# Kernel tuning notes

Measured on AMD Instinct MI355X. Metric: run time of the kernel, lower is better.

## Reference

```python
import jax, jax.numpy as jnp
import numpy as np

SENTINEL = 24635
NUM_ENTITIES = 24636
EMB_DIM = 128


def setup_inputs() -> dict:
    key = jax.random.key(0)
    ks = jax.random.split(key, 6)
    B, L = 4096, 50
    return {
        "encoded_context_embs": jax.random.normal(ks[0], (B, 1024), jnp.float32),
        "ent_embs": jax.random.normal(ks[1], (NUM_ENTITIES, EMB_DIM), jnp.float32) * 0.02,
        "W1": jax.random.normal(ks[2], (768, 1024), jnp.float32) * 0.02,
        "W2": jax.random.normal(ks[3], (512, 768), jnp.float32) * 0.02,
        "W3": jax.random.normal(ks[4], (128, 512), jnp.float32) * 0.02,
        "ent_list": jax.random.randint(ks[5], (B, L), 0, NUM_ENTITIES, jnp.int64),
    }


def reference(encoded_context_embs, ent_embs, W1, W2, W3, ent_list):
    # --- ragged gather + masked mean with sentinel early-exit ---
    # valid[b, l] == 1 iff no sentinel appeared at positions <= l (prefix-AND)
    not_sent = (ent_list != SENTINEL).astype(ent_embs.dtype)   # [B, L]
    valid = jnp.cumprod(not_sent, axis=1)                      # [B, L]
    gathered = ent_embs[ent_list]                              # [B, L, D]
    cnt = valid.sum(axis=1)                                    # [B]
    summed = jnp.einsum("bl,bld->bd", valid, gathered)        # [B, D]
    mean = summed / jnp.maximum(cnt, 1.0)[:, None]
    # sentinel at position 0 -> fall back to the sentinel embedding
    user_embs = jnp.where((cnt == 0)[:, None], ent_embs[SENTINEL][None, :], mean)

    # --- MLP on pooled context: 1024 -> 768 -> 512 -> 128 ---
    x = jax.nn.relu(encoded_context_embs @ W1.T)
    x = jax.nn.relu(x @ W2.T)
    q = x @ W3.T                                               # [B, 128]

    # --- cross attention: query=q, key=value=user_embs ---
    scale = 1.0 / jnp.sqrt(jnp.asarray(q.shape[-1], q.dtype))
    scores = (q @ user_embs.T) * scale                         # [B, B]
    weights = jax.nn.softmax(scores, axis=-1)
    return weights @ user_embs                                 # [B, 128]
```

## Files before the change

### kernel.cpp

```cpp
#include <hip/hip_runtime.h>
#include <hip/hip_bf16.h>

#define SENTINEL 24635

typedef unsigned char f8_t;
using bf16x8  = __attribute__((ext_vector_type(8))) __bf16;
using bf16x2  = __attribute__((ext_vector_type(2))) __bf16;
using floatx4 = __attribute__((ext_vector_type(4))) float;

__device__ inline int pack4_fp8(float4 a, float s) {
  int w = __builtin_amdgcn_cvt_pk_fp8_f32(a.x * s, a.y * s, 0, false);
  return __builtin_amdgcn_cvt_pk_fp8_f32(a.z * s, a.w * s, w, true);
}

__device__ inline void store_fp8x8(f8_t* d, float4 a, float4 b, float s) {
  int2 v; v.x = pack4_fp8(a, s); v.y = pack4_fp8(b, s);
  *(int2*)d = v;
}

__device__ inline void gll16(const void* g, void* l) {
  __builtin_amdgcn_global_load_lds(
      (const __attribute__((address_space(1))) unsigned int*)g,
      (__attribute__((address_space(3))) unsigned int*)l, 16, 0, 0);
}

__global__ __launch_bounds__(256) void prep_kernel(
    const float* __restrict__ s0, f8_t* __restrict__ d0,
    const float* __restrict__ s1, f8_t* __restrict__ d1,
    const float* __restrict__ s2, f8_t* __restrict__ d2,
    const float* __restrict__ s3, f8_t* __restrict__ d3,
    const float* __restrict__ ent, const int* __restrict__ ent_list,
    __bf16* __restrict__ user_n) {
  if (blockIdx.x < 2656) {
    int g = blockIdx.x * 256 + threadIdx.x;
    const float* s; f8_t* d; int i; float sc;
    if (g < 524288)      { s = s0; d = d0; i = g;          sc = 1.f;  }
    else if (g < 622592) { s = s1; d = d1; i = g - 524288; sc = 16.f; }
    else if (g < 671744) { s = s2; d = d2; i = g - 622592; sc = 16.f; }
    else if (g < 679936) { s = s3; d = d3; i = g - 671744; sc = 16.f; }
    else return;
    i *= 8;
    float4 a = *(const float4*)(s + i);
    float4 b = *(const float4*)(s + i + 4);
    store_fp8x8(d + i, a, b, sc);
    return;
  }
  const int b = (blockIdx.x - 2656) * 4 + (threadIdx.x >> 6);
  const int lane = threadIdx.x & 63;
  int myidx = (lane < 50) ? ent_list[b * 50 + lane] : 0;
  unsigned long long m = __ballot(lane < 50 && myidx == SENTINEL);
  const int cnt = (m == 0) ? 50 : (int)__builtin_ctzll(m);

  float sx = 0.f, sy = 0.f;
  for (int l0 = 0; l0 < 50; l0 += 10) {
    if (l0 >= cnt) break;
    float2 e[10];
#pragma unroll
    for (int j = 0; j < 10; ++j) {
      int idx = __shfl(myidx, l0 + j);
      e[j] = *(const float2*)(ent + (size_t)idx * 128 + lane * 2);
    }
#pragma unroll
    for (int j = 0; j < 10; ++j) {
      if (l0 + j < cnt) { sx += e[j].x; sy += e[j].y; }
    }
  }
  float vx, vy;
  if (cnt == 0) {
    float2 e = *(const float2*)(ent + (size_t)SENTINEL * 128 + lane * 2);
    vx = e.x; vy = e.y;
  } else {
    float inv = 1.f / (float)cnt;
    vx = sx * inv; vy = sy * inv;
  }
  bf16x2 o; o[0] = (__bf16)vx; o[1] = (__bf16)vy;
  *(bf16x2*)(user_n + (size_t)b * 128 + lane * 2) = o;
}

template <int WR, int WC, int MT, int NT, int RELU, bool OUT_BF16>
__device__ inline void gemm_body_f8(const f8_t* __restrict__ A,
                                    const f8_t* __restrict__ W,
                                    void* __restrict__ Cout,
                                    int M, int N, int K, int bn0, int bm0,
                                    char* lds) {
  constexpr int BM = WR * MT * 16;
  constexpr int BN = WC * NT * 16;
  auto As = (f8_t (*)[BM][32])lds;
  auto Bs = (f8_t (*)[BN][32])(lds + (size_t)2 * BM * 32);
  const int tid  = threadIdx.x;
  const int w    = tid >> 6;
  const int lane = tid & 63;
  const int quad = lane >> 4;
  const int l16  = lane & 15;
  const int wr   = w / WC;
  const int wc   = w % WC;
  const int lrow = lane >> 1;
  const int lcol = (lane & 1) * 16;

  floatx4 acc[MT][NT];
#pragma unroll
  for (int mt = 0; mt < MT; ++mt)
#pragma unroll
    for (int nt = 0; nt < NT; ++nt) acc[mt][nt] = (floatx4){0.f, 0.f, 0.f, 0.f};

  constexpr int nAc = 2 * (BM / 32);
  constexpr int nBc = 2 * (BN / 32);
  for (int k0 = 0; k0 < K; k0 += 64) {
    __syncthreads();
#pragma unroll
    for (int c = w; c < nAc; c += 4) {
      int s = c / (BM / 32);
      int r = (c % (BM / 32)) * 32;
      gll16(A + (size_t)(bm0 + r + lrow) * K + k0 + s * 32 + lcol, &As[s][r][0]);
    }
#pragma unroll
    for (int c = w; c < nBc; c += 4) {
      int s = c / (BN / 32);
      int r = (c % (BN / 32)) * 32;
      gll16(W + (size_t)(bn0 + r + lrow) * K + k0 + s * 32 + lcol, &Bs[s][r][0]);
    }
    __syncthreads();
#pragma unroll
    for (int s = 0; s < 2; ++s) {
      long af[MT], bfr[NT];
#pragma unroll
      for (int mt = 0; mt < MT; ++mt)
        af[mt] = *(const long*)&As[s][wr * (MT * 16) + mt * 16 + l16][quad * 8];
#pragma unroll
      for (int nt = 0; nt < NT; ++nt)
        bfr[nt] = *(const long*)&Bs[s][wc * (NT * 16) + nt * 16 + l16][quad * 8];
#pragma unroll
      for (int mt = 0; mt < MT; ++mt)
#pragma unroll
        for (int nt = 0; nt < NT; ++nt)
          acc[mt][nt] = __builtin_amdgcn_mfma_f32_16x16x32_fp8_fp8(
              af[mt], bfr[nt], acc[mt][nt], 0, 0, 0);
    }
  }

  const float osc = 0.0625f;
#pragma unroll
  for (int mt = 0; mt < MT; ++mt) {
    const int row0 = bm0 + wr * (MT * 16) + mt * 16 + quad * 4;
#pragma unroll
    for (int nt = 0; nt < NT; ++nt) {
      const int col = bn0 + wc * (NT * 16) + nt * 16 + l16;
#pragma unroll
      for (int r = 0; r < 4; ++r) {
        float v = acc[mt][nt][r] * osc;
        if (RELU) v = fmaxf(v, 0.f);
        if (OUT_BF16) {
          ((__bf16*)Cout)[(size_t)(row0 + r) * N + col] = (__bf16)v;
        } else {
          int p = __builtin_amdgcn_cvt_pk_fp8_f32(v, v, 0, false);
          ((f8_t*)Cout)[(size_t)(row0 + r) * N + col] = (f8_t)(p & 0xff);
        }
      }
    }
  }
}

template <int WR, int WC, int MT, int NT, int RELU, bool OUT_BF16>
__global__ __launch_bounds__(256) void gemm_f8(const f8_t* __restrict__ A,
                                               const f8_t* __restrict__ W,
                                               void* __restrict__ C,
                                               int M, int N, int K) {
  __shared__ char lds[(size_t)2 * ((WR * MT * 16) + (WC * NT * 16)) * 32];
  gemm_body_f8<WR, WC, MT, NT, RELU, OUT_BF16>(
      A, W, C, M, N, K, blockIdx.x * (WC * NT * 16), blockIdx.y * (WR * MT * 16),
      lds);
}

__global__ __launch_bounds__(256) void gemm1_tr(const f8_t* __restrict__ A,
                                                const f8_t* __restrict__ W,
                                                f8_t* __restrict__ C,
                                                const __bf16* __restrict__ un,
                                                __bf16* __restrict__ ut) {
  __shared__ char lds[10240];
  const int bx = blockIdx.x;
  if (bx < 512) {
    gemm_body_f8<2, 2, 2, 3, 1, false>(A, W, C, 4096, 768, 1024,
                                       (bx % 8) * 96, (bx / 8) * 64, lds);
    return;
  }
  const int idx = bx - 512;
  const int r0 = (idx & 63) * 64;
  const int c0 = (idx >> 6) * 64;
  auto T = (__bf16 (*)[72])lds;
  const int tid = threadIdx.x;
#pragma unroll
  for (int p = 0; p < 2; ++p) {
    int r = (tid >> 3) + p * 32;
    int c = (tid & 7) * 8;
    *(bf16x8*)&T[r][c] = *(const bf16x8*)(un + (size_t)(r0 + r) * 128 + c0 + c);
  }
  __syncthreads();
#pragma unroll
  for (int p = 0; p < 2; ++p) {
    int c = (tid >> 3) + p * 32;
    int r = (tid & 7) * 8;
    bf16x8 v;
#pragma unroll
    for (int j = 0; j < 8; ++j) v[j] = T[r + j][c];
    *(bf16x8*)(ut + (size_t)(c0 + c) * 4096 + r0 + r) = v;
  }
}

__global__ __launch_bounds__(256) void flash_attn(const __bf16* __restrict__ Q,
                                                  const __bf16* __restrict__ Un_g,
                                                  const __bf16* __restrict__ Ut_g,
                                                  __bf16* __restrict__ O_part,
                                                  float* __restrict__ lp) {
  __shared__ __bf16 Un[64][136];
  __shared__ __bf16 Ut[128][72];
  __shared__ __bf16 Ps[4][32][72];
  const int tid  = threadIdx.x;
  const int w    = tid >> 6;
  const int lane = tid & 63;
  const int quad = lane >> 4;
  const int l16  = lane & 15;
  const int qrow0 = blockIdx.x * 128;
  const int split = blockIdx.y;
  const float scale = 0.08838834764831845f;

  bf16x8 aq[2][4];
#pragma unroll
  for (int mt = 0; mt < 2; ++mt)
#pragma unroll
    for (int c = 0; c < 4; ++c)
      aq[mt][c] = *(const bf16x8*)(Q + (size_t)(qrow0 + w * 32 + mt * 16 + l16) * 128 +
                                   c * 32 + quad * 8);

  floatx4 o[2][8];
#pragma unroll
  for (int mt = 0; mt < 2; ++mt)
#pragma unroll
    for (int t = 0; t < 8; ++t) o[mt][t] = (floatx4){0.f, 0.f, 0.f, 0.f};
  float lsum[2][4] = {{0.f, 0.f, 0.f, 0.f}, {0.f, 0.f, 0.f, 0.f}};

  for (int chunk = 0; chunk < 4; ++chunk) {
    const int key0 = (split * 4 + chunk) * 64;
    __syncthreads();
#pragma unroll
    for (int p = 0; p < 4; ++p) {
      int r = (tid >> 4) + p * 16;
      int c = (tid & 15) * 8;
      *(bf16x8*)&Un[r][c] = *(const bf16x8*)(Un_g + (size_t)(key0 + r) * 128 + c);
    }
#pragma unroll
    for (int p = 0; p < 4; ++p) {
      int d = (tid >> 3) + p * 32;
      int kk = (tid & 7) * 8;
      *(bf16x8*)&Ut[d][kk] = *(const bf16x8*)(Ut_g + (size_t)d * 4096 + key0 + kk);
    }
    __syncthreads();

#pragma unroll
    for (int t = 0; t < 4; ++t) {
      bf16x8 bk[4];
#pragma unroll
      for (int c = 0; c < 4; ++c)
        bk[c] = *(const bf16x8*)&Un[t * 16 + l16][c * 32 + quad * 8];
      floatx4 s0 = (floatx4){0.f, 0.f, 0.f, 0.f};
      floatx4 s1 = (floatx4){0.f, 0.f, 0.f, 0.f};
#pragma unroll
      for (int c = 0; c < 4; ++c) {
        s0 = __builtin_amdgcn_mfma_f32_16x16x32_bf16(aq[0][c], bk[c], s0, 0, 0, 0);
        s1 = __builtin_amdgcn_mfma_f32_16x16x32_bf16(aq[1][c], bk[c], s1, 0, 0, 0);
      }
#pragma unroll
      for (int r = 0; r < 4; ++r) {
        float p0 = __expf(s0[r] * scale);
        float p1 = __expf(s1[r] * scale);
        lsum[0][r] += p0;
        lsum[1][r] += p1;
        Ps[w][quad * 4 + r][t * 16 + l16] = (__bf16)p0;
        Ps[w][16 + quad * 4 + r][t * 16 + l16] = (__bf16)p1;
      }
    }

#pragma unroll
    for (int c2 = 0; c2 < 2; ++c2) {
      bf16x8 ap0 = *(const bf16x8*)&Ps[w][l16][c2 * 32 + quad * 8];
      bf16x8 ap1 = *(const bf16x8*)&Ps[w][16 + l16][c2 * 32 + quad * 8];
#pragma unroll
      for (int dt = 0; dt < 8; ++dt) {
        bf16x8 bv = *(const bf16x8*)&Ut[dt * 16 + l16][c2 * 32 + quad * 8];
        o[0][dt] = __builtin_amdgcn_mfma_f32_16x16x32_bf16(ap0, bv, o[0][dt], 0, 0, 0);
        o[1][dt] = __builtin_amdgcn_mfma_f32_16x16x32_bf16(ap1, bv, o[1][dt], 0, 0, 0);
      }
    }
  }

#pragma unroll
  for (int mt = 0; mt < 2; ++mt)
#pragma unroll
    for (int r = 0; r < 4; ++r) {
      float v = lsum[mt][r];
      v += __shfl_xor(v, 1);
      v += __shfl_xor(v, 2);
      v += __shfl_xor(v, 4);
      v += __shfl_xor(v, 8);
      lsum[mt][r] = v;
    }

  __bf16* Ob = O_part + (size_t)split * 524288;
#pragma unroll
  for (int mt = 0; mt < 2; ++mt) {
    const int row0 = qrow0 + w * 32 + mt * 16 + quad * 4;
#pragma unroll
    for (int dt = 0; dt < 8; ++dt) {
#pragma unroll
      for (int r = 0; r < 4; ++r) {
        Ob[(size_t)(row0 + r) * 128 + dt * 16 + l16] = (__bf16)o[mt][dt][r];
      }
    }
    if (l16 == 0) {
#pragma unroll
      for (int r = 0; r < 4; ++r) lp[(size_t)split * 4096 + row0 + r] = lsum[mt][r];
    }
  }
}

__global__ __launch_bounds__(256) void combine_kernel(const __bf16* __restrict__ Op,
                                                      const float* __restrict__ lp,
                                                      float* __restrict__ out) {
  const int i = (blockIdx.x * 256 + threadIdx.x) * 8;
  const int row = i >> 7;
  float num[8] = {0.f, 0.f, 0.f, 0.f, 0.f, 0.f, 0.f, 0.f};
  float den = 0.f;
#pragma unroll
  for (int s = 0; s < 16; ++s) {
    bf16x8 v = *(const bf16x8*)(Op + (size_t)s * 524288 + i);
#pragma unroll
    for (int j = 0; j < 8; ++j) num[j] += (float)v[j];
    den += lp[(size_t)s * 4096 + row];
  }
  float inv = 1.f / den;
  float4 r0 = {num[0] * inv, num[1] * inv, num[2] * inv, num[3] * inv};
  float4 r1 = {num[4] * inv, num[5] * inv, num[6] * inv, num[7] * inv};
  *(float4*)(out + i) = r0;
  *(float4*)(out + i + 4) = r1;
}

extern "C" void kernel_launch(void* const* d_in, const int* in_sizes, int n_in,
                              void* d_out, int out_size, void* d_ws, size_t ws_size,
                              hipStream_t stream) {
  (void)in_sizes; (void)n_in; (void)out_size; (void)ws_size;
  const float* ctx      = (const float*)d_in[0];
  const float* ent_embs = (const float*)d_in[1];
  const float* W1       = (const float*)d_in[2];
  const float* W2       = (const float*)d_in[3];
  const float* W3       = (const float*)d_in[4];
  const int*   ent_list = (const int*)d_in[5];
  float* out = (float*)d_out;

  char* base = (char*)d_ws;
  __bf16* user_n = (__bf16*)(base);
  __bf16* user_t = (__bf16*)(base + (1ull << 20));
  __bf16* qb     = (__bf16*)(base + (2ull << 20));
  float*  lp     = (float*)(base + (3ull << 20));
  f8_t*   ctxb   = (f8_t*)(base + (4ull << 20));
  f8_t*   W1b    = (f8_t*)(base + (8ull << 20));
  f8_t*   W2b    = (f8_t*)(base + 9175040ull);
  f8_t*   W3b    = (f8_t*)(base + 9568256ull);
  f8_t*   x1b    = (f8_t*)(base + (10ull << 20));
  f8_t*   x2b    = (f8_t*)(base + (13ull << 20));
  __bf16* O_part = (__bf16*)(base + (15ull << 20));

  prep_kernel<<<3680, 256, 0, stream>>>(ctx, ctxb, W1, W1b, W2, W2b, W3, W3b,
                                        ent_embs, ent_list, user_n);
  gemm1_tr<<<640, 256, 0, stream>>>(ctxb, W1b, x1b, user_n, user_t);
  gemm_f8<2, 2, 2, 2, 1, false><<<dim3(8, 64), 256, 0, stream>>>(
      x1b, W2b, x2b, 4096, 512, 768);
  gemm_f8<2, 2, 1, 1, 0, true><<<dim3(4, 128), 256, 0, stream>>>(
      x2b, W3b, qb, 4096, 128, 512);
  flash_attn<<<dim3(32, 16), 256, 0, stream>>>(qb, user_n, user_t, O_part, lp);
  combine_kernel<<<256, 256, 0, stream>>>(O_part, lp, out);
}
```

Baseline: 156.2 us.

## Prefetch attention key chunks into registers and move W2/W3 conversion into gemm1

The flash-attention loop now loads the next 64-key chunk of Un/Ut from global memory into registers while computing on the current chunk, then stores it to LDS after a barrier. This hides global load latency behind the MFMA work. MFMA sections are wrapped in s_setprio raises. The W2/W3 fp8 conversion moves from the prep kernel into extra blocks of the gemm1 launch, shrinking prep and overlapping that conversion with the first GEMM. The cost is higher register pressure from the prefetch buffers and an extra barrier per chunk.

```diff
diff --git a/kernel.cpp b/kernel.cpp
--- a/kernel.cpp
+++ b/kernel.cpp
@@ -27,25 +27,20 @@
 __global__ __launch_bounds__(256) void prep_kernel(
     const float* __restrict__ s0, f8_t* __restrict__ d0,
     const float* __restrict__ s1, f8_t* __restrict__ d1,
-    const float* __restrict__ s2, f8_t* __restrict__ d2,
-    const float* __restrict__ s3, f8_t* __restrict__ d3,
     const float* __restrict__ ent, const int* __restrict__ ent_list,
     __bf16* __restrict__ user_n) {
-  if (blockIdx.x < 2656) {
+  if (blockIdx.x < 2432) {
     int g = blockIdx.x * 256 + threadIdx.x;
     const float* s; f8_t* d; int i; float sc;
     if (g < 524288)      { s = s0; d = d0; i = g;          sc = 1.f;  }
-    else if (g < 622592) { s = s1; d = d1; i = g - 524288; sc = 16.f; }
-    else if (g < 671744) { s = s2; d = d2; i = g - 622592; sc = 16.f; }
-    else if (g < 679936) { s = s3; d = d3; i = g - 671744; sc = 16.f; }
-    else return;
+    else                 { s = s1; d = d1; i = g - 524288; sc = 16.f; }
     i *= 8;
     float4 a = *(const float4*)(s + i);
     float4 b = *(const float4*)(s + i + 4);
     store_fp8x8(d + i, a, b, sc);
     return;
   }
-  const int b = (blockIdx.x - 2656) * 4 + (threadIdx.x >> 6);
+  const int b = (blockIdx.x - 2432) * 4 + (threadIdx.x >> 6);
   const int lane = threadIdx.x & 63;
   int myidx = (lane < 50) ? ent_list[b * 50 + lane] : 0;
   unsigned long long m = __ballot(lane < 50 && myidx == SENTINEL);
@@ -175,12 +170,27 @@
                                                 const f8_t* __restrict__ W,
                                                 f8_t* __restrict__ C,
                                                 const __bf16* __restrict__ un,
-                                                __bf16* __restrict__ ut) {
+                                                __bf16* __restrict__ ut,
+                                                const float* __restrict__ s2,
+                                                f8_t* __restrict__ d2,
+                                                const float* __restrict__ s3,
+                                                f8_t* __restrict__ d3) {
   __shared__ char lds[10240];
   const int bx = blockIdx.x;
   if (bx < 512) {
     gemm_body_f8<2, 2, 2, 3, 1, false>(A, W, C, 4096, 768, 1024,
                                        (bx % 8) * 96, (bx / 8) * 64, lds);
+    return;
+  }
+  if (bx >= 640) {
+    int g = (bx - 640) * 256 + threadIdx.x;
+    const float* s; f8_t* d; int i;
+    if (g < 49152) { s = s2; d = d2; i = g; }
+    else           { s = s3; d = d3; i = g - 49152; }
+    i *= 8;
+    float4 a = *(const float4*)(s + i);
+    float4 b = *(const float4*)(s + i + 4);
+    store_fp8x8(d + i, a, b, 16.f);
     return;
   }
   const int idx = bx - 512;
@@ -238,22 +248,34 @@
     for (int t = 0; t < 8; ++t) o[mt][t] = (floatx4){0.f, 0.f, 0.f, 0.f};
   float lsum[2][4] = {{0.f, 0.f, 0.f, 0.f}, {0.f, 0.f, 0.f, 0.f}};
 
+  const int sr = tid >> 4, sc = (tid & 15) * 8;
+  const int td = tid >> 3, tk = (tid & 7) * 8;
+  bf16x8 un_r[4], ut_r[4];
+
+#define LD_CHUNK(key0)                                                         \
+  do {                                                                         \
+    _Pragma("unroll")                                                          \
+    for (int p = 0; p < 4; ++p)                                                \
+      un_r[p] = *(const bf16x8*)(Un_g + (size_t)((key0) + sr + p * 16) * 128 + sc); \
+    _Pragma("unroll")                                                          \
+    for (int p = 0; p < 4; ++p)                                                \
+      ut_r[p] = *(const bf16x8*)(Ut_g + (size_t)(td + p * 32) * 4096 + (key0) + tk); \
+  } while (0)
+
+#define ST_CHUNK()                                                             \
+  do {                                                                         \
+    _Pragma("unroll")                                                          \
+    for (int p = 0; p < 4; ++p) *(bf16x8*)&Un[sr + p * 16][sc] = un_r[p];      \
+    _Pragma("unroll")                                                          \
+    for (int p = 0; p < 4; ++p) *(bf16x8*)&Ut[td + p * 32][tk] = ut_r[p];      \
+  } while (0)
+
+  LD_CHUNK(split * 256);
+  ST_CHUNK();
+  __syncthreads();
+
   for (int chunk = 0; chunk < 4; ++chunk) {
-    const int key0 = (split * 4 + chunk) * 64;
-    __syncthreads();
-#pragma unroll
-    for (int p = 0; p < 4; ++p) {
-      int r = (tid >> 4) + p * 16;
-      int c = (tid & 15) * 8;
-      *(bf16x8*)&Un[r][c] = *(const bf16x8*)(Un_g + (size_t)(key0 + r) * 128 + c);
-    }
-#pragma unroll
-    for (int p = 0; p < 4; ++p) {
-      int d = (tid >> 3) + p * 32;
-      int kk = (tid & 7) * 8;
-      *(bf16x8*)&Ut[d][kk] = *(const bf16x8*)(Ut_g + (size_t)d * 4096 + key0 + kk);
-    }
-    __syncthreads();
+    if (chunk < 3) LD_CHUNK(split * 256 + (chunk + 1) * 64);
 
 #pragma unroll
     for (int t = 0; t < 4; ++t) {
@@ -263,11 +285,13 @@
         bk[c] = *(const bf16x8*)&Un[t * 16 + l16][c * 32 + quad * 8];
       floatx4 s0 = (floatx4){0.f, 0.f, 0.f, 0.f};
       floatx4 s1 = (floatx4){0.f, 0.f, 0.f, 0.f};
+      __builtin_amdgcn_s_setprio(1);
 #pragma unroll
       for (int c = 0; c < 4; ++c) {
         s0 = __builtin_amdgcn_mfma_f32_16x16x32_bf16(aq[0][c], bk[c], s0, 0, 0, 0);
         s1 = __builtin_amdgcn_mfma_f32_16x16x32_bf16(aq[1][c], bk[c], s1, 0, 0, 0);
       }
+      __builtin_amdgcn_s_setprio(0);
 #pragma unroll
       for (int r = 0; r < 4; ++r) {
         float p0 = __expf(s0[r] * scale);
@@ -283,14 +307,24 @@
     for (int c2 = 0; c2 < 2; ++c2) {
       bf16x8 ap0 = *(const bf16x8*)&Ps[w][l16][c2 * 32 + quad * 8];
       bf16x8 ap1 = *(const bf16x8*)&Ps[w][16 + l16][c2 * 32 + quad * 8];
+      __builtin_amdgcn_s_setprio(1);
 #pragma unroll
       for (int dt = 0; dt < 8; ++dt) {
         bf16x8 bv = *(const bf16x8*)&Ut[dt * 16 + l16][c2 * 32 + quad * 8];
         o[0][dt] = __builtin_amdgcn_mfma_f32_16x16x32_bf16(ap0, bv, o[0][dt], 0, 0, 0);
         o[1][dt] = __builtin_amdgcn_mfma_f32_16x16x32_bf16(ap1, bv, o[1][dt], 0, 0, 0);
       }
-    }
-  }
+      __builtin_amdgcn_s_setprio(0);
+    }
+
+    __syncthreads();
+    if (chunk < 3) {
+      ST_CHUNK();
+      __syncthreads();
+    }
+  }
+#undef LD_CHUNK
+#undef ST_CHUNK
 
 #pragma unroll
   for (int mt = 0; mt < 2; ++mt)
@@ -368,9 +402,10 @@
   f8_t*   x2b    = (f8_t*)(base + (13ull << 20));
   __bf16* O_part = (__bf16*)(base + (15ull << 20));
 
-  prep_kernel<<<3680, 256, 0, stream>>>(ctx, ctxb, W1, W1b, W2, W2b, W3, W3b,
+  prep_kernel<<<3456, 256, 0, stream>>>(ctx, ctxb, W1, W1b,
                                         ent_embs, ent_list, user_n);
-  gemm1_tr<<<640, 256, 0, stream>>>(ctxb, W1b, x1b, user_n, user_t);
+  gemm1_tr<<<864, 256, 0, stream>>>(ctxb, W1b, x1b, user_n, user_t,
+                                    W2, W2b, W3, W3b);
   gemm_f8<2, 2, 2, 2, 1, false><<<dim3(8, 64), 256, 0, stream>>>(
       x1b, W2b, x2b, 4096, 512, 768);
   gemm_f8<2, 2, 1, 1, 0, true><<<dim3(4, 128), 256, 0, stream>>>(
```

New measurement: 148.5 us. -4.9%, faster.
